# Kernel optimization log

Measured on AMD Instinct MI355X. Metric: run time of the kernel, lower is better.

Reference implementation:

```python
import jax, jax.numpy as jnp
import numpy as np

B, T, D = 4, 2048, 768
H = 12
DH = D // H
DFF = 3072
EPS = 1e-5


def _layernorm(x, g, b):
    mu = jnp.mean(x, axis=-1, keepdims=True)
    var = jnp.var(x, axis=-1, keepdims=True)
    return (x - mu) * jax.lax.rsqrt(var + EPS) * g + b


def setup_inputs() -> dict:
    key = jax.random.key(0)
    ks = jax.random.split(key, 12)
    s = lambda fan_in: 1.0 / np.sqrt(fan_in)
    return {
        "x": jax.random.normal(ks[0], (B, T, D), dtype=jnp.float32),
        "ln1_g": jnp.ones((D,), jnp.float32),
        "ln1_b": jnp.zeros((D,), jnp.float32),
        "w_qkv": jax.random.uniform(ks[1], (D, 3 * D), jnp.float32, -s(D), s(D)),
        "b_qkv": jax.random.uniform(ks[2], (3 * D,), jnp.float32, -s(D), s(D)),
        "w_proj": jax.random.uniform(ks[3], (D, D), jnp.float32, -s(D), s(D)),
        "b_proj": jax.random.uniform(ks[4], (D,), jnp.float32, -s(D), s(D)),
        "ln2_g": jnp.ones((D,), jnp.float32),
        "ln2_b": jnp.zeros((D,), jnp.float32),
        "w_ff1": jax.random.uniform(ks[5], (D, DFF), jnp.float32, -s(D), s(D)),
        "b_ff1": jax.random.uniform(ks[6], (DFF,), jnp.float32, -s(D), s(D)),
        "w_ff2": jax.random.uniform(ks[7], (DFF, D), jnp.float32, -s(DFF), s(DFF)),
        "b_ff2": jax.random.uniform(ks[8], (D,), jnp.float32, -s(DFF), s(DFF)),
    }


def reference(x, ln1_g, ln1_b, w_qkv, b_qkv, w_proj, b_proj,
              ln2_g, ln2_b, w_ff1, b_ff1, w_ff2, b_ff2):
    # --- attention sublayer ---
    h = _layernorm(x, ln1_g, ln1_b)
    qkv = h @ w_qkv + b_qkv                       # [B,T,3D]
    q, k, v = jnp.split(qkv, 3, axis=-1)
    q = q.reshape(B, T, H, DH).transpose(0, 2, 1, 3)  # [B,H,T,DH]
    k = k.reshape(B, T, H, DH).transpose(0, 2, 1, 3)
    v = v.reshape(B, T, H, DH).transpose(0, 2, 1, 3)
    att = jnp.einsum('bhqd,bhkd->bhqk', q, k) / jnp.sqrt(jnp.float32(DH))
    causal = jnp.tril(jnp.ones((T, T), dtype=bool))
    att = jnp.where(causal, att, -jnp.inf)
    att = jax.nn.softmax(att, axis=-1)
    out = jnp.einsum('bhqk,bhkd->bhqd', att, v)    # [B,H,T,DH]
    out = out.transpose(0, 2, 1, 3).reshape(B, T, D)
    x = x + out @ w_proj + b_proj
    # --- MLP sublayer ---
    h2 = _layernorm(x, ln2_g, ln2_b)
    h2 = jax.nn.gelu(h2 @ w_ff1 + b_ff1, approximate=False)
    x = x + h2 @ w_ff2 + b_ff2
    return x
```

## Files before the change

kernel.cpp:

```cpp
#include <hip/hip_runtime.h>
#include <cstdint>
#include <cstddef>

typedef unsigned short u16;
typedef unsigned int u32;
typedef __attribute__((ext_vector_type(8))) short s16x8;
typedef __attribute__((ext_vector_type(4))) float f32x4;

#define NB 4
#define NT 2048
#define ND 768
#define NH 12
#define NDH 64
#define NFF 3072
#define NM (NB*NT)

__device__ __forceinline__ u16 f2b(float f){
  union { float f; unsigned u; } c; c.f = f;
  unsigned r = c.u + 0x7fffu + ((c.u >> 16) & 1u);
  return (u16)(r >> 16);
}

__device__ __forceinline__ f32x4 mfma16(s16x8 a, s16x8 b, f32x4 c){
  return __builtin_amdgcn_mfma_f32_16x16x32_bf16(a, b, c, 0, 0, 0);
}

__device__ __forceinline__ void stage16(u16* lds, const u16* g){
  __builtin_amdgcn_global_load_lds(
      (const __attribute__((address_space(1))) unsigned int*)g,
      (__attribute__((address_space(3))) unsigned int*)lds,
      16, 0, 0);
}

__global__ __launch_bounds__(256) void transpose_bf16(
    const float* __restrict__ in, u16* __restrict__ out, int K, int N)
{
  __shared__ float tile[32][33];
  const int n0 = blockIdx.x * 32, k0 = blockIdx.y * 32;
  const int tx = threadIdx.x, ty = threadIdx.y;
  #pragma unroll
  for (int i = 0; i < 32; i += 8)
    tile[ty + i][tx] = in[(size_t)(k0 + ty + i) * N + n0 + tx];
  __syncthreads();
  #pragma unroll
  for (int i = 0; i < 32; i += 8)
    out[(size_t)(n0 + ty + i) * K + k0 + tx] = f2b(tile[tx][ty + i]);
}

__global__ __launch_bounds__(256) void ln_kernel(
    const float* __restrict__ x, const float* __restrict__ g,
    const float* __restrict__ b, u16* __restrict__ out)
{
  const int row = blockIdx.x;
  const int t = threadIdx.x;
  const float* xr = x + (size_t)row * ND;
  float v0 = xr[t], v1 = xr[t + 256], v2 = xr[t + 512];
  float s = v0 + v1 + v2;
  float ss = v0*v0 + v1*v1 + v2*v2;
  #pragma unroll
  for (int o = 32; o; o >>= 1) { s += __shfl_xor(s, o, 64); ss += __shfl_xor(ss, o, 64); }
  __shared__ float red[8];
  const int w = t >> 6;
  if ((t & 63) == 0) { red[w] = s; red[4 + w] = ss; }
  __syncthreads();
  s  = red[0] + red[1] + red[2] + red[3];
  ss = red[4] + red[5] + red[6] + red[7];
  const float mu = s * (1.f / ND);
  const float var = ss * (1.f / ND) - mu * mu;
  const float rinv = rsqrtf(var + 1e-5f);
  u16* orow = out + (size_t)row * ND;
  orow[t]       = f2b((v0 - mu) * rinv * g[t]       + b[t]);
  orow[t + 256] = f2b((v1 - mu) * rinv * g[t + 256] + b[t + 256]);
  orow[t + 512] = f2b((v2 - mu) * rinv * g[t + 512] + b[t + 512]);
}

template<int EPI>
__global__ __launch_bounds__(256,4) void gemm_bt(
    const u16* __restrict__ A, const u16* __restrict__ Bt,
    const float* __restrict__ bias, const float* __restrict__ res,
    void* __restrict__ o0, void* __restrict__ o1, void* __restrict__ o2,
    const int M, const int N, const int K)
{
  __shared__ u16 As[128 * 32];
  __shared__ u16 Bs[128 * 32];
  const int tid = threadIdx.x;
  const int lane = tid & 63, wid = tid >> 6;
  const int wr = wid >> 1, wc = wid & 1;
  const int lg = lane >> 4, lm = lane & 15;
  const int bm = blockIdx.x * 128, bn = blockIdx.y * 128;

  f32x4 acc[4][4] = {};

  const u16* ApT = A  + (size_t)(bm + (tid >> 2)) * K + (tid & 3) * 8;
  const u16* BpT = Bt + (size_t)(bn + (tid >> 2)) * K + (tid & 3) * 8;
  u16* AsW = &As[wid * 512];
  u16* BsW = &Bs[wid * 512];
  const size_t rowStride64 = (size_t)64 * K;

  for (int k0 = 0; k0 < K; k0 += 32) {
    __syncthreads();
    stage16(AsW,        ApT + k0);
    stage16(AsW + 2048, ApT + rowStride64 + k0);
    stage16(BsW,        BpT + k0);
    stage16(BsW + 2048, BpT + rowStride64 + k0);
    __syncthreads();
    s16x8 af[4], bf[4];
    #pragma unroll
    for (int i = 0; i < 4; i++) af[i] = *(const s16x8*)&As[(wr * 64 + i * 16 + lm) * 32 + lg * 8];
    #pragma unroll
    for (int j = 0; j < 4; j++) bf[j] = *(const s16x8*)&Bs[(wc * 64 + j * 16 + lm) * 32 + lg * 8];
    #pragma unroll
    for (int i = 0; i < 4; i++)
      #pragma unroll
      for (int j = 0; j < 4; j++)
        acc[i][j] = mfma16(af[i], bf[j], acc[i][j]);
  }

  #pragma unroll
  for (int i = 0; i < 4; i++)
    #pragma unroll
    for (int j = 0; j < 4; j++) {
      const int col = bn + wc * 64 + j * 16 + lm;
      const float bb = bias[col];
      #pragma unroll
      for (int r = 0; r < 4; r++) {
        const int row = bm + wr * 64 + i * 16 + lg * 4 + r;
        float v = acc[i][j][r] + bb;
        if (EPI == 0) {
          u16* dst; int rem;
          if (col < ND)            { dst = (u16*)o0; rem = col; v *= 0.125f; }
          else if (col < 2 * ND)   { dst = (u16*)o1; rem = col - ND; }
          else                     { dst = (u16*)o2; rem = col - 2 * ND; }
          const int hh = rem >> 6, dh = rem & 63;
          const int bb2 = row >> 11, tt = row & 2047;
          dst[(((size_t)bb2 * NH + hh) * NT + tt) * NDH + dh] = f2b(v);
        } else if (EPI == 1) {
          ((float*)o0)[(size_t)row * ND + col] = v + res[(size_t)row * ND + col];
        } else if (EPI == 2) {
          const float ge = 0.5f * v * (1.f + erff(v * 0.70710678118654752f));
          ((u16*)o0)[(size_t)row * NFF + col] = f2b(ge);
        } else {
          ((float*)o0)[(size_t)row * ND + col] = v + res[(size_t)row * ND + col];
        }
      }
    }
}

__global__ __launch_bounds__(256,2) void attn_kernel(
    const u16* __restrict__ Q, const u16* __restrict__ Kg,
    const u16* __restrict__ V, u16* __restrict__ O)
{
  const int pairIdx = blockIdx.x;
  const int bh = blockIdx.y;
  const int b = bh / NH, h = bh % NH;
  const int tid = threadIdx.x;
  const int lane = tid & 63, w = tid >> 6;
  const int lg = lane >> 4, lm = lane & 15;
  const int sr = tid >> 3;
  const int sc = (tid & 7) * 8;

  __shared__ u16 Ks[64 * 64];
  __shared__ u16 Vt[64 * 64];
  __shared__ u16 Ps[4][16 * 64];

  const u16* Qb = Q  + (size_t)bh * NT * NDH;
  const u16* Kb = Kg + (size_t)bh * NT * NDH;
  const u16* Vb = V  + (size_t)bh * NT * NDH;

  for (int half = 0; half < 2; ++half) {
    const int si = half ? (31 - pairIdx) : pairIdx;
    const int q0 = si * 64;
    const int ktmax = si;

    const s16x8 qf0 = *(const s16x8*)&Qb[(size_t)(q0 + w * 16 + lm) * NDH + lg * 8];
    const s16x8 qf1 = *(const s16x8*)&Qb[(size_t)(q0 + w * 16 + lm) * NDH + 32 + lg * 8];

    f32x4 oacc[4] = {};
    float m = -INFINITY, l = 0.f;

    s16x8 kva = *(const s16x8*)&Kb[(size_t)sr * NDH + sc];
    s16x8 kvb = *(const s16x8*)&Kb[(size_t)(sr + 32) * NDH + sc];
    s16x8 vva = *(const s16x8*)&Vb[(size_t)sr * NDH + sc];
    s16x8 vvb = *(const s16x8*)&Vb[(size_t)(sr + 32) * NDH + sc];

    for (int kt = 0; kt <= ktmax; ++kt) {
      __syncthreads();
      *(s16x8*)&Ks[sr * 64 + (sc ^ ((sr & 7) << 3))] = kva;
      *(s16x8*)&Ks[(sr + 32) * 64 + (sc ^ ((sr & 7) << 3))] = kvb;
      #pragma unroll
      for (int e = 0; e < 8; ++e)
        Vt[(sc + e) * 64 + (sr ^ ((tid & 7) << 3))] = (u16)vva[e];
      #pragma unroll
      for (int e = 0; e < 8; ++e)
        Vt[(sc + e) * 64 + ((sr + 32) ^ ((tid & 7) << 3))] = (u16)vvb[e];
      __syncthreads();

      if (kt < ktmax) {
        const u16* Kn = Kb + (size_t)(kt + 1) * 64 * NDH;
        const u16* Vn = Vb + (size_t)(kt + 1) * 64 * NDH;
        kva = *(const s16x8*)&Kn[(size_t)sr * NDH + sc];
        kvb = *(const s16x8*)&Kn[(size_t)(sr + 32) * NDH + sc];
        vva = *(const s16x8*)&Vn[(size_t)sr * NDH + sc];
        vvb = *(const s16x8*)&Vn[(size_t)(sr + 32) * NDH + sc];
      }

      f32x4 sv[4];
      #pragma unroll
      for (int n = 0; n < 4; ++n) {
        const int krow = (n * 16 + lm) * 64;
        const int swz = (lm & 7) << 3;
        s16x8 kf0 = *(const s16x8*)&Ks[krow + ((lg * 8) ^ swz)];
        s16x8 kf1 = *(const s16x8*)&Ks[krow + ((32 + lg * 8) ^ swz)];
        f32x4 s4 = {};
        s4 = mfma16(kf0, qf0, s4);
        s4 = mfma16(kf1, qf1, s4);
        sv[n] = s4;
      }

      if (kt == ktmax) {
        #pragma unroll
        for (int n = 0; n < 4; ++n)
          #pragma unroll
          for (int r = 0; r < 4; ++r)
            if (n * 16 + lg * 4 + r > w * 16 + lm) sv[n][r] = -INFINITY;
      }

      float mx = -INFINITY;
      #pragma unroll
      for (int n = 0; n < 4; ++n)
        #pragma unroll
        for (int r = 0; r < 4; ++r) mx = fmaxf(mx, sv[n][r]);
      mx = fmaxf(mx, __shfl_xor(mx, 16));
      mx = fmaxf(mx, __shfl_xor(mx, 32));
      const float mnew = fmaxf(m, mx);
      const float alpha = __expf(m - mnew);
      m = mnew;

      float rs = 0.f;
      u32 pk[4][2];
      #pragma unroll
      for (int n = 0; n < 4; ++n) {
        const float p0 = __expf(sv[n][0] - mnew);
        const float p1 = __expf(sv[n][1] - mnew);
        const float p2 = __expf(sv[n][2] - mnew);
        const float p3 = __expf(sv[n][3] - mnew);
        rs += (p0 + p1) + (p2 + p3);
        pk[n][0] = (u32)f2b(p0) | ((u32)f2b(p1) << 16);
        pk[n][1] = (u32)f2b(p2) | ((u32)f2b(p3) << 16);
      }
      rs += __shfl_xor(rs, 16);
      rs += __shfl_xor(rs, 32);
      l = l * alpha + rs;

      #pragma unroll
      for (int n = 0; n < 4; ++n) {
        const int idx0 = lm * 64 + ((n * 16 + lg * 4) ^ ((lm & 7) << 3));
        *(u32*)&Ps[w][idx0] = pk[n][0];
        *(u32*)&Ps[w][idx0 + 2] = pk[n][1];
      }

      float av[4];
      #pragma unroll
      for (int r = 0; r < 4; ++r) av[r] = __shfl(alpha, lg * 4 + r);
      #pragma unroll
      for (int d = 0; d < 4; ++d)
        #pragma unroll
        for (int r = 0; r < 4; ++r) oacc[d][r] *= av[r];

      #pragma unroll
      for (int kh = 0; kh < 2; ++kh) {
        const s16x8 pf = *(const s16x8*)&Ps[w][lm * 64 + ((kh * 32 + lg * 8) ^ ((lm & 7) << 3))];
        #pragma unroll
        for (int dt = 0; dt < 4; ++dt) {
          const int g = (2 * dt + (lm >> 3)) & 7;
          const s16x8 vf = *(const s16x8*)&Vt[(dt * 16 + lm) * 64 + (((kh * 4 + lg) ^ g) << 3)];
          oacc[dt] = mfma16(pf, vf, oacc[dt]);
        }
      }
    }

    float lv[4];
    #pragma unroll
    for (int r = 0; r < 4; ++r) lv[r] = 1.f / __shfl(l, lg * 4 + r);
    #pragma unroll
    for (int dt = 0; dt < 4; ++dt)
      #pragma unroll
      for (int r = 0; r < 4; ++r) {
        const int qg = q0 + w * 16 + lg * 4 + r;
        O[((size_t)b * NT + qg) * ND + h * NDH + dt * 16 + lm] = f2b(oacc[dt][r] * lv[r]);
      }
  }
}

extern "C" void kernel_launch(void* const* d_in, const int* in_sizes, int n_in,
                              void* d_out, int out_size, void* d_ws, size_t ws_size,
                              hipStream_t stream)
{
  const float* x      = (const float*)d_in[0];
  const float* ln1_g  = (const float*)d_in[1];
  const float* ln1_b  = (const float*)d_in[2];
  const float* w_qkv  = (const float*)d_in[3];
  const float* b_qkv  = (const float*)d_in[4];
  const float* w_proj = (const float*)d_in[5];
  const float* b_proj = (const float*)d_in[6];
  const float* ln2_g  = (const float*)d_in[7];
  const float* ln2_b  = (const float*)d_in[8];
  const float* w_ff1  = (const float*)d_in[9];
  const float* b_ff1  = (const float*)d_in[10];
  const float* w_ff2  = (const float*)d_in[11];
  const float* b_ff2  = (const float*)d_in[12];

  char* ws = (char*)d_ws;
  u16*   wt_qkv = (u16*)(ws + 0);
  u16*   wt_proj= (u16*)(ws + 3538944);
  u16*   wt_ff1 = (u16*)(ws + 4718592);
  u16*   wt_ff2 = (u16*)(ws + 9437184);
  u16*   hbuf   = (u16*)(ws + 14155776);
  u16*   qbuf   = (u16*)(ws + 26738688);
  u16*   kbuf   = (u16*)(ws + 39321600);
  u16*   vbuf   = (u16*)(ws + 51904512);
  u16*   aobuf  = (u16*)(ws + 64487424);
  float* x1     = (float*)(ws + 77070336);
  u16*   h2buf  = (u16*)(ws + 102236160);
  u16*   ff1buf = hbuf;

  transpose_bf16<<<dim3(2304/32,  768/32), dim3(32,8), 0, stream>>>(w_qkv,  wt_qkv,  768, 2304);
  transpose_bf16<<<dim3( 768/32,  768/32), dim3(32,8), 0, stream>>>(w_proj, wt_proj, 768,  768);
  transpose_bf16<<<dim3(3072/32,  768/32), dim3(32,8), 0, stream>>>(w_ff1,  wt_ff1,  768, 3072);
  transpose_bf16<<<dim3( 768/32, 3072/32), dim3(32,8), 0, stream>>>(w_ff2,  wt_ff2, 3072,  768);

  ln_kernel<<<NM, 256, 0, stream>>>(x, ln1_g, ln1_b, hbuf);
  gemm_bt<0><<<dim3(NM/128, 2304/128), 256, 0, stream>>>(hbuf, wt_qkv, b_qkv, nullptr,
                                                         qbuf, kbuf, vbuf, NM, 2304, ND);
  attn_kernel<<<dim3(16, NB*NH), 256, 0, stream>>>(qbuf, kbuf, vbuf, aobuf);
  gemm_bt<1><<<dim3(NM/128, ND/128), 256, 0, stream>>>(aobuf, wt_proj, b_proj, x,
                                                       x1, nullptr, nullptr, NM, ND, ND);
  ln_kernel<<<NM, 256, 0, stream>>>(x1, ln2_g, ln2_b, h2buf);
  gemm_bt<2><<<dim3(NM/128, NFF/128), 256, 0, stream>>>(h2buf, wt_ff1, b_ff1, nullptr,
                                                        ff1buf, nullptr, nullptr, NM, NFF, ND);
  gemm_bt<3><<<dim3(NM/128, ND/128), 256, 0, stream>>>(ff1buf, wt_ff2, b_ff2, x1,
                                                       d_out, nullptr, nullptr, NM, ND, NFF);
}
```

Baseline: 305.1 us.

## Double-buffer GEMM shared-memory tiles to overlap loads with MFMA

The GEMM main loop now uses two shared-memory buffers for the A and B tiles. It prefetches the next K-tile into the alternate buffer while computing on the current one, which removes one of the two barriers per iteration. Shared memory per block doubles to 32KB, which may lower occupancy under launch_bounds(256,4). stage16 appears to be a direct global-to-LDS copy, so the load and the MFMA work can overlap.

Result: no change. 306.8 us (+0.6%).

```diff
diff --git a/kernel.cpp b/kernel.cpp
--- a/kernel.cpp
+++ b/kernel.cpp
@@ -81,8 +81,8 @@
     void* __restrict__ o0, void* __restrict__ o1, void* __restrict__ o2,
     const int M, const int N, const int K)
 {
-  __shared__ u16 As[128 * 32];
-  __shared__ u16 Bs[128 * 32];
+  __shared__ u16 As[2][128 * 32];
+  __shared__ u16 Bs[2][128 * 32];
   const int tid = threadIdx.x;
   const int lane = tid & 63, wid = tid >> 6;
   const int wr = wid >> 1, wc = wid & 1;
@@ -93,22 +93,42 @@
 
   const u16* ApT = A  + (size_t)(bm + (tid >> 2)) * K + (tid & 3) * 8;
   const u16* BpT = Bt + (size_t)(bn + (tid >> 2)) * K + (tid & 3) * 8;
-  u16* AsW = &As[wid * 512];
-  u16* BsW = &Bs[wid * 512];
-  const size_t rowStride64 = (size_t)64 * K;
-
-  for (int k0 = 0; k0 < K; k0 += 32) {
+  const size_t rs64 = (size_t)64 * K;
+  const int woff = wid * 512;
+
+  stage16(&As[0][woff],        ApT);
+  stage16(&As[0][woff + 2048], ApT + rs64);
+  stage16(&Bs[0][woff],        BpT);
+  stage16(&Bs[0][woff + 2048], BpT + rs64);
+  __syncthreads();
+
+  int cur = 0;
+  const int nt = K >> 5;
+  for (int t = 1; t < nt; ++t) {
+    const int k0 = t << 5;
+    stage16(&As[cur ^ 1][woff],        ApT + k0);
+    stage16(&As[cur ^ 1][woff + 2048], ApT + rs64 + k0);
+    stage16(&Bs[cur ^ 1][woff],        BpT + k0);
+    stage16(&Bs[cur ^ 1][woff + 2048], BpT + rs64 + k0);
+    s16x8 af[4], bf[4];
+    #pragma unroll
+    for (int i = 0; i < 4; i++) af[i] = *(const s16x8*)&As[cur][(wr * 64 + i * 16 + lm) * 32 + lg * 8];
+    #pragma unroll
+    for (int j = 0; j < 4; j++) bf[j] = *(const s16x8*)&Bs[cur][(wc * 64 + j * 16 + lm) * 32 + lg * 8];
+    #pragma unroll
+    for (int i = 0; i < 4; i++)
+      #pragma unroll
+      for (int j = 0; j < 4; j++)
+        acc[i][j] = mfma16(af[i], bf[j], acc[i][j]);
     __syncthreads();
-    stage16(AsW,        ApT + k0);
-    stage16(AsW + 2048, ApT + rowStride64 + k0);
-    stage16(BsW,        BpT + k0);
-    stage16(BsW + 2048, BpT + rowStride64 + k0);
-    __syncthreads();
+    cur ^= 1;
+  }
+  {
     s16x8 af[4], bf[4];
     #pragma unroll
-    for (int i = 0; i < 4; i++) af[i] = *(const s16x8*)&As[(wr * 64 + i * 16 + lm) * 32 + lg * 8];
-    #pragma unroll
-    for (int j = 0; j < 4; j++) bf[j] = *(const s16x8*)&Bs[(wc * 64 + j * 16 + lm) * 32 + lg * 8];
+    for (int i = 0; i < 4; i++) af[i] = *(const s16x8*)&As[cur][(wr * 64 + i * 16 + lm) * 32 + lg * 8];
+    #pragma unroll
+    for (int j = 0; j < 4; j++) bf[j] = *(const s16x8*)&Bs[cur][(wc * 64 + j * 16 + lm) * 32 + lg * 8];
     #pragma unroll
     for (int i = 0; i < 4; i++)
       #pragma unroll
```
